# Kernel optimization log

Hardware: AMD Instinct MI355X
Metric: run time of the kernel (lower is better)

## Reference

```python
import jax, jax.numpy as jnp
import numpy as np

N = 50000        # num nodes
E = 800000       # num edges (no self loops by construction)
D = 128          # in_features == out_features
NE = 4           # num_envs
EPS = 1e-8
STDV = 1.0 / np.sqrt(D)


def setup_inputs() -> dict:
    key = jax.random.key(0)
    k = jax.random.split(key, 6)
    x = jax.random.normal(k[0], (N, D), jnp.float32)
    row = jax.random.randint(k[1], (E,), 0, N, dtype=jnp.int32)
    off = jax.random.randint(k[2], (E,), 1, N, dtype=jnp.int32)
    col = (row + off) % N  # guarantees no self loops (matches remove_self_loops)
    adj = jnp.stack([row, col])
    env_weights = jax.random.uniform(k[3], (N, NE), jnp.float32)
    weights = jax.random.uniform(k[4], (NE, D, D), jnp.float32, -STDV, STDV)
    a = jax.random.normal(k[5], (NE, 2 * D, 1), jnp.float32) * np.sqrt(2.0 / (2 * D + 1)) * 1.414
    return {"x": x, "adj": adj, "env_weights": env_weights, "weights": weights, "a": a}


def reference(x, adj, env_weights, weights, a):
    n = x.shape[0]
    f = weights.shape[-1]
    loops = jnp.arange(n, dtype=adj.dtype)
    src = jnp.concatenate([adj[0], loops])  # add_self_loops
    dst = jnp.concatenate([adj[1], loops])
    # per-env projected features: [NE, N, F]
    h = jnp.einsum('nd,edf->enf', x, weights)
    # attention logits: cat(h[src], h[dst]) @ a  ==  h[src]@a1 + h[dst]@a2
    a1 = a[:, :f, 0]   # [NE, F]
    a2 = a[:, f:, 0]   # [NE, F]
    s_src = jnp.einsum('enf,ef->en', h, a1)
    s_dst = jnp.einsum('enf,ef->en', h, a2)
    logits = jax.nn.leaky_relu(s_src[:, src] + s_dst[:, dst], 0.01)  # [NE, Etot]
    # global per-env max subtraction (as in the torch code: max over all edges)
    e = jnp.exp(logits - jnp.max(logits, axis=1, keepdims=True))
    def agg(ek, hk):
        # specialspmm: out[src] += ek * hk[dst]; denom via ones vector
        denom = jax.ops.segment_sum(ek, src, num_segments=n) + EPS          # [N]
        num = jax.ops.segment_sum(ek[:, None] * hk[dst], src, num_segments=n)  # [N, F]
        return num / denom[:, None]
    out_env = jax.vmap(agg)(e, h)  # [NE, N, F]
    out = jnp.einsum('ne,enf->nf', env_weights, out_env)
    return out + x  # residual
```

## Files before the change

kernel.cpp:

```cpp
#include <hip/hip_runtime.h>

#define N_NODES 50000
#define N_EDGES 800000
#define D_FEAT  128
#define NE_ENV  4
#define EPS_F   1e-8f
#define M_CONST 4.0f
#define SCAN_NB 196
#define NB_BUCKET 391
#define BINA_EPT 16

typedef __attribute__((ext_vector_type(8))) short bf16x8;
typedef __attribute__((ext_vector_type(4))) float floatx4;
typedef __attribute__((ext_vector_type(2))) float f32x2;

static __device__ __forceinline__ unsigned short f2bf(float v) {
    union { float f; unsigned int u; } c; c.f = v;
    unsigned int u = c.u;
    u += 0x7fffu + ((u >> 16) & 1u);
    return (unsigned short)(u >> 16);
}

static __device__ __forceinline__ f32x2 bf2f(unsigned int v) {
    f32x2 r;
    r.x = __uint_as_float(v << 16);
    r.y = __uint_as_float(v & 0xffff0000u);
    return r;
}

static __device__ __forceinline__ float lrelu_exp(float z) {
    float lk = z > 0.f ? z : 0.01f * z;
    return __expf(lk - M_CONST);
}

static __device__ __forceinline__ void pk_add(f32x2& acc, f32x2 w) {
    asm("v_pk_add_f32 %0, %1, %0" : "+v"(acc) : "v"(w));
}
static __device__ __forceinline__ void pk_fma_bl(f32x2& acc, f32x2 w, f32x2 x) {
    asm("v_pk_fma_f32 %0, %1, %2, %0 op_sel:[0,0,0] op_sel_hi:[0,1,1]" : "+v"(acc) : "v"(w), "v"(x));
}
static __device__ __forceinline__ void pk_fma_bh(f32x2& acc, f32x2 w, f32x2 x) {
    asm("v_pk_fma_f32 %0, %1, %2, %0 op_sel:[1,0,0] op_sel_hi:[1,1,1]" : "+v"(acc) : "v"(w), "v"(x));
}

static __device__ __forceinline__ void edge_acc(unsigned int xv, float4 w,
        f32x2& den01, f32x2& den23, f32x2* axy) {
    f32x2 x = bf2f(xv);
    f32x2 wxy; wxy.x = w.x; wxy.y = w.y;
    f32x2 wzw; wzw.x = w.z; wzw.y = w.w;
    pk_add(den01, wxy);
    pk_add(den23, wzw);
    pk_fma_bl(axy[0], wxy, x);
    pk_fma_bh(axy[1], wxy, x);
    pk_fma_bl(axy[2], wzw, x);
    pk_fma_bh(axy[3], wzw, x);
}

__global__ __launch_bounds__(256) void k_setup(const float* __restrict__ weights, const float* __restrict__ a,
        float* __restrict__ b, unsigned short* __restrict__ wsw,
        const int* __restrict__ row, int* __restrict__ counts) {
    int blk = blockIdx.x;
    if (blk < 128) {
        int wave = threadIdx.x >> 6, lane = threadIdx.x & 63;
        int t = blk * 4 + wave;
        int e = t >> 7, d = t & 127;
        float2 w2 = ((const float2*)(weights + e * 16384 + d * 128))[lane];
        float2 a1 = ((const float2*)(a + e * 256))[lane];
        float2 a2 = ((const float2*)(a + e * 256 + 128))[lane];
        float p1 = w2.x * a1.x + w2.y * a1.y;
        float p2 = w2.x * a2.x + w2.y * a2.y;
#pragma unroll
        for (int off = 32; off > 0; off >>= 1) {
            p1 += __shfl_xor(p1, off, 64);
            p2 += __shfl_xor(p2, off, 64);
        }
        if (lane == 0) {
            b[e * 128 + d] = p1;
            b[512 + e * 128 + d] = p2;
        }
    } else if (blk < 384) {
        int idx = (blk - 128) * 256 + threadIdx.x;
        int j = idx & 7;
        int l = (idx >> 3) & 63;
        int t = (idx >> 9) & 7;
        int s = idx >> 12;
        int k = s * 32 + (l >> 4) * 8 + j;
        int f = t * 16 + (l & 15);
        int e = k >> 7, d = k & 127;
        wsw[idx] = f2bf(weights[e * 16384 + d * 128 + f]);
    } else {
        int k = (blk - 384) * 256 + threadIdx.x;
        if (k < N_EDGES) atomicAdd(&counts[row[k]], 1);
    }
}

__global__ __launch_bounds__(256) void k_s(const float* __restrict__ x, const float* __restrict__ b,
        float* __restrict__ s_src, float* __restrict__ s_dst, unsigned short* __restrict__ xbf) {
    int wave = threadIdx.x >> 6, lane = threadIdx.x & 63;
    int gw = blockIdx.x * 4 + wave;
    if (gw >= 3125) return;
    int quad = lane >> 4, lm = lane & 15;
    int base = gw * 16;

    floatx4 acc = (floatx4){0.f, 0.f, 0.f, 0.f};
    const float* xrow = x + (size_t)(base + lm) * 128 + quad * 8;
    unsigned short* xbrow = xbf + (size_t)(base + lm) * 128 + quad * 8;

#pragma unroll
    for (int s = 0; s < 4; ++s) {
        float4 lo = *(const float4*)(xrow + s * 32);
        float4 hi = *(const float4*)(xrow + s * 32 + 4);
        bf16x8 af;
        af[0] = (short)f2bf(lo.x); af[1] = (short)f2bf(lo.y);
        af[2] = (short)f2bf(lo.z); af[3] = (short)f2bf(lo.w);
        af[4] = (short)f2bf(hi.x); af[5] = (short)f2bf(hi.y);
        af[6] = (short)f2bf(hi.z); af[7] = (short)f2bf(hi.w);
        *(bf16x8*)(xbrow + s * 32) = af;

        bf16x8 bfv = (bf16x8){0, 0, 0, 0, 0, 0, 0, 0};
        if (lm < 8) {
            const float* bp = b + lm * 128 + s * 32 + quad * 8;
            float4 b0 = *(const float4*)bp;
            float4 b1 = *(const float4*)(bp + 4);
            bfv[0] = (short)f2bf(b0.x); bfv[1] = (short)f2bf(b0.y);
            bfv[2] = (short)f2bf(b0.z); bfv[3] = (short)f2bf(b0.w);
            bfv[4] = (short)f2bf(b1.x); bfv[5] = (short)f2bf(b1.y);
            bfv[6] = (short)f2bf(b1.z); bfv[7] = (short)f2bf(b1.w);
        }
        acc = __builtin_amdgcn_mfma_f32_16x16x32_bf16(af, bfv, acc, 0, 0, 0);
    }
    if (lm < 8) {
        float* dstp = (lm < 4) ? (s_src + (size_t)(base + quad * 4) * 4 + lm)
                               : (s_dst + (size_t)(base + quad * 4) * 4 + (lm - 4));
#pragma unroll
        for (int r = 0; r < 4; ++r) dstp[r * 4] = acc[r];
    }
}

__global__ void k_scan_a(const int* __restrict__ counts, int* __restrict__ partial) {
    __shared__ int sm[256];
    int idx = blockIdx.x * 256 + threadIdx.x;
    sm[threadIdx.x] = (idx < N_NODES) ? counts[idx] : 0;
    __syncthreads();
    for (int s = 128; s > 0; s >>= 1) {
        if (threadIdx.x < s) sm[threadIdx.x] += sm[threadIdx.x + s];
        __syncthreads();
    }
    if (threadIdx.x == 0) partial[blockIdx.x] = sm[0];
}

__global__ void k_scan_b(const int* __restrict__ partial, int* __restrict__ chunk_off) {
    __shared__ int sm[256];
    int t = threadIdx.x;
    int v = (t < SCAN_NB) ? partial[t] : 0;
    sm[t] = v;
    __syncthreads();
    for (int s2 = 1; s2 < 256; s2 <<= 1) {
        int add = (t >= s2) ? sm[t - s2] : 0;
        __syncthreads();
        sm[t] += add;
        __syncthreads();
    }
    chunk_off[t] = sm[t] - v;
}

__global__ void k_scan_c(const int* __restrict__ counts, const int* __restrict__ chunk_off,
                         int* __restrict__ offsets, int* __restrict__ bcur) {
    __shared__ int sm[256];
    int t = threadIdx.x;
    int idx = blockIdx.x * 256 + t;
    int v = (idx < N_NODES) ? counts[idx] : 0;
    sm[t] = v;
    __syncthreads();
    for (int s2 = 1; s2 < 256; s2 <<= 1) {
        int add = (t >= s2) ? sm[t - s2] : 0;
        __syncthreads();
        sm[t] += add;
        __syncthreads();
    }
    if (idx < N_NODES) {
        int excl = chunk_off[blockIdx.x] + sm[t] - v;
        offsets[idx] = excl;
        if ((idx & 127) == 0) bcur[idx >> 7] = excl;
    }
    if (idx == 0) offsets[N_NODES] = N_EDGES;
}

__global__ __launch_bounds__(256) void k_binA(const int* __restrict__ row, const int* __restrict__ col,
        int* __restrict__ bcur, unsigned int* __restrict__ binned) {
    __shared__ int cnt[NB_BUCKET];
    __shared__ int base[NB_BUCKET];
    int t = threadIdx.x;
    for (int b = t; b < NB_BUCKET; b += 256) cnt[b] = 0;
    __syncthreads();
    unsigned int pk[BINA_EPT];
    int ebase = blockIdx.x * (256 * BINA_EPT) + t;
#pragma unroll
    for (int j = 0; j < BINA_EPT; ++j) {
        int k = ebase + j * 256;
        pk[j] = 0xffffffffu;
        if (k < N_EDGES) {
            unsigned int s = (unsigned int)row[k];
            unsigned int d = (unsigned int)col[k];
            pk[j] = (s << 16) | d;
            atomicAdd(&cnt[s >> 7], 1);
        }
    }
    __syncthreads();
    for (int b = t; b < NB_BUCKET; b += 256) {
        int c = cnt[b];
        base[b] = c ? atomicAdd(&bcur[b], c) : 0;
        cnt[b] = 0;
    }
    __syncthreads();
#pragma unroll
    for (int j = 0; j < BINA_EPT; ++j) {
        if (pk[j] != 0xffffffffu) {
            int b = pk[j] >> 23;
            int off = atomicAdd(&cnt[b], 1);
            binned[base[b] + off] = pk[j];
        }
    }
}

__global__ __launch_bounds__(256) void k_binB(const unsigned int* __restrict__ binned,
        const int* __restrict__ offsets,
        const float* __restrict__ s_src, const float* __restrict__ s_dst,
        int* __restrict__ sorted_dst, float4* __restrict__ w_sorted) {
    __shared__ int cur[128];
    int b = blockIdx.x;
    int nb = b << 7;
    int nc = min(128, N_NODES - nb);
    int t = threadIdx.x;
    if (t < nc) cur[t] = offsets[nb + t];
    __syncthreads();
    int ebeg = offsets[nb];
    int eend = offsets[nb + nc];
    for (int i = ebeg + t; i < eend; i += 256) {
        unsigned int pk = binned[i];
        int s = (int)(pk >> 16), d = (int)(pk & 0xffffu);
        float4 a4 = *(const float4*)(s_src + s * 4);
        float4 b4 = *(const float4*)(s_dst + d * 4);
        float4 w;
        w.x = lrelu_exp(a4.x + b4.x);
        w.y = lrelu_exp(a4.y + b4.y);
        w.z = lrelu_exp(a4.z + b4.z);
        w.w = lrelu_exp(a4.w + b4.w);
        int pos = atomicAdd(&cur[s - nb], 1);
        sorted_dst[pos] = d;
        w_sorted[pos] = w;
    }
}

__global__ __launch_bounds__(256) void k_agg(const unsigned int* __restrict__ xb,
        const float* __restrict__ s_src, const float* __restrict__ s_dst,
        const int* __restrict__ offsets, const int* __restrict__ sorted_dst,
        const float4* __restrict__ w_sorted, const float* __restrict__ env_w,
        unsigned short* __restrict__ Gp) {
    int wave = threadIdx.x >> 6, lane = threadIdx.x & 63;
    int n = blockIdx.x * 4 + wave;
    if (n >= N_NODES) return;

    f32x2 den01, den23;
    f32x2 axy[4];

    {
        float4 sa = *(const float4*)(s_src + n * 4);
        float4 sb = *(const float4*)(s_dst + n * 4);
        float ws0 = lrelu_exp(sa.x + sb.x), ws1 = lrelu_exp(sa.y + sb.y);
        float ws2 = lrelu_exp(sa.z + sb.z), ws3 = lrelu_exp(sa.w + sb.w);
        f32x2 xv = bf2f(xb[((unsigned)n << 6) + lane]);
        den01.x = ws0; den01.y = ws1;
        den23.x = ws2; den23.y = ws3;
        axy[0].x = ws0 * xv.x; axy[0].y = ws0 * xv.y;
        axy[1].x = ws1 * xv.x; axy[1].y = ws1 * xv.y;
        axy[2].x = ws2 * xv.x; axy[2].y = ws2 * xv.y;
        axy[3].x = ws3 * xv.x; axy[3].y = ws3 * xv.y;
    }

    int beg = __builtin_amdgcn_readfirstlane(offsets[n]);
    int end = __builtin_amdgcn_readfirstlane(offsets[n + 1]);
    int i = beg;
    for (; i + 7 < end; i += 8) {
        int d[8]; float4 w[8]; unsigned int v[8];
#pragma unroll
        for (int j = 0; j < 8; ++j) d[j] = sorted_dst[i + j];
#pragma unroll
        for (int j = 0; j < 8; ++j) v[j] = xb[((unsigned)d[j] << 6) + lane];
#pragma unroll
        for (int j = 0; j < 8; ++j) w[j] = w_sorted[i + j];
#pragma unroll
        for (int j = 0; j < 8; ++j) edge_acc(v[j], w[j], den01, den23, axy);
    }
    for (; i + 3 < end; i += 4) {
        int d[4]; float4 w[4]; unsigned int v[4];
#pragma unroll
        for (int j = 0; j < 4; ++j) d[j] = sorted_dst[i + j];
#pragma unroll
        for (int j = 0; j < 4; ++j) v[j] = xb[((unsigned)d[j] << 6) + lane];
#pragma unroll
        for (int j = 0; j < 4; ++j) w[j] = w_sorted[i + j];
#pragma unroll
        for (int j = 0; j < 4; ++j) edge_acc(v[j], w[j], den01, den23, axy);
    }
    for (; i < end; ++i) {
        int d0 = sorted_dst[i];
        edge_acc(xb[((unsigned)d0 << 6) + lane], w_sorted[i], den01, den23, axy);
    }

    float4 ewt = *(const float4*)(env_w + n * 4);
    float ewv[4] = { ewt.x, ewt.y, ewt.z, ewt.w };
    float dens[4] = { den01.x, den01.y, den23.x, den23.y };
    unsigned int* grow = (unsigned int*)(Gp + (size_t)n * 512);
#pragma unroll
    for (int e = 0; e < 4; ++e) {
        float sc = ewv[e] / (dens[e] + EPS_F);
        unsigned int lo = f2bf(sc * axy[e].x);
        unsigned int hi = f2bf(sc * axy[e].y);
        grow[e * 64 + lane] = (hi << 16) | lo;
    }
}

__global__ __launch_bounds__(256) void k_gemm(const unsigned short* __restrict__ Gp,
        const unsigned short* __restrict__ Wsw,
        const float* __restrict__ x, float* __restrict__ out) {
    int wave = threadIdx.x >> 6, lane = threadIdx.x & 63;
    int gw = blockIdx.x * 4 + wave;
    if (gw >= 3125) return;
    int quad = lane >> 4, lm = lane & 15;
    int m = gw * 16 + lm;

    floatx4 acc[8];
#pragma unroll
    for (int t = 0; t < 8; ++t) acc[t] = (floatx4){0.f, 0.f, 0.f, 0.f};

    const unsigned short* Arow = Gp + (size_t)m * 512 + quad * 8;
#pragma unroll
    for (int s = 0; s < 16; ++s) {
        bf16x8 af = *(const bf16x8*)(Arow + s * 32);
#pragma unroll
        for (int t = 0; t < 8; ++t) {
            bf16x8 bfv = *(const bf16x8*)(Wsw + (((s * 8 + t) * 64 + lane) * 8));
            acc[t] = __builtin_amdgcn_mfma_f32_16x16x32_bf16(af, bfv, acc[t], 0, 0, 0);
        }
    }
    int row_base = gw * 16 + quad * 4;
#pragma unroll
    for (int t = 0; t < 8; ++t) {
        int colc = t * 16 + lm;
#pragma unroll
        for (int r = 0; r < 4; ++r) {
            int rowi = row_base + r;
            out[rowi * 128 + colc] = acc[t][r] + x[rowi * 128 + colc];
        }
    }
}

extern "C" void kernel_launch(void* const* d_in, const int* in_sizes, int n_in,
                              void* d_out, int out_size, void* d_ws, size_t ws_size,
                              hipStream_t stream) {
    const float* x       = (const float*)d_in[0];
    const int*   adj     = (const int*)d_in[1];
    const int*   row     = adj;
    const int*   col     = adj + N_EDGES;
    const float* env_w   = (const float*)d_in[2];
    const float* weights = (const float*)d_in[3];
    const float* a       = (const float*)d_in[4];
    float* out = (float*)d_out;

    char* ws = (char*)d_ws;
    size_t off = 0;
    auto alloc = [&](size_t bytes) -> char* {
        char* p = ws + off;
        off += (bytes + 255) & ~(size_t)255;
        return p;
    };
    float* b          = (float*)alloc(1024 * 4);
    float* s_src      = (float*)alloc((size_t)N_NODES * 4 * 4);
    float* s_dst      = (float*)alloc((size_t)N_NODES * 4 * 4);
    int*   counts     = (int*)alloc((size_t)N_NODES * 4);
    int*   offsets    = (int*)alloc((size_t)(N_NODES + 1) * 4);
    int*   partial    = (int*)alloc(256 * 4);
    int*   chunk_off  = (int*)alloc(256 * 4);
    int*   bcur       = (int*)alloc(512 * 4);
    unsigned int* binned = (unsigned int*)alloc((size_t)N_EDGES * 4);
    int*   sorted_dst = (int*)alloc((size_t)N_EDGES * 4);
    float4* w_sorted  = (float4*)alloc((size_t)N_EDGES * 16);
    unsigned short* wsw = (unsigned short*)alloc(65536 * 2);
    unsigned short* xbf = (unsigned short*)alloc((size_t)N_NODES * 128 * 2);
    unsigned short* Gp  = (unsigned short*)alloc((size_t)N_NODES * 512 * 2);

    hipMemsetAsync(counts, 0, (size_t)N_NODES * 4, stream);
    k_setup<<<3509, 256, 0, stream>>>(weights, a, b, wsw, row, counts);
    k_s<<<782, 256, 0, stream>>>(x, b, s_src, s_dst, xbf);
    k_scan_a<<<SCAN_NB, 256, 0, stream>>>(counts, partial);
    k_scan_b<<<1, 256, 0, stream>>>(partial, chunk_off);
    k_scan_c<<<SCAN_NB, 256, 0, stream>>>(counts, chunk_off, offsets, bcur);
    k_binA<<<196, 256, 0, stream>>>(row, col, bcur, binned);
    k_binB<<<NB_BUCKET, 256, 0, stream>>>(binned, offsets, s_src, s_dst, sorted_dst, w_sorted);
    k_agg<<<12500, 256, 0, stream>>>((const unsigned int*)xbf, s_src, s_dst, offsets, sorted_dst, w_sorted, env_w, Gp);
    k_gemm<<<782, 256, 0, stream>>>(Gp, wsw, x, out);
}
```

Measured before the change: 228.5 us.

## Fuse aggregation and output GEMM via shared-memory tile

```diff
diff --git a/kernel.cpp b/kernel.cpp
--- a/kernel.cpp
+++ b/kernel.cpp
@@ -252,107 +252,103 @@
     }
 }
 
-__global__ __launch_bounds__(256) void k_agg(const unsigned int* __restrict__ xb,
+__global__ __launch_bounds__(256) void k_agg_gemm(const unsigned int* __restrict__ xb,
         const float* __restrict__ s_src, const float* __restrict__ s_dst,
         const int* __restrict__ offsets, const int* __restrict__ sorted_dst,
         const float4* __restrict__ w_sorted, const float* __restrict__ env_w,
-        unsigned short* __restrict__ Gp) {
-    int wave = threadIdx.x >> 6, lane = threadIdx.x & 63;
-    int n = blockIdx.x * 4 + wave;
-    if (n >= N_NODES) return;
-
-    f32x2 den01, den23;
-    f32x2 axy[4];
-
-    {
-        float4 sa = *(const float4*)(s_src + n * 4);
-        float4 sb = *(const float4*)(s_dst + n * 4);
-        float ws0 = lrelu_exp(sa.x + sb.x), ws1 = lrelu_exp(sa.y + sb.y);
-        float ws2 = lrelu_exp(sa.z + sb.z), ws3 = lrelu_exp(sa.w + sb.w);
-        f32x2 xv = bf2f(xb[((unsigned)n << 6) + lane]);
-        den01.x = ws0; den01.y = ws1;
-        den23.x = ws2; den23.y = ws3;
-        axy[0].x = ws0 * xv.x; axy[0].y = ws0 * xv.y;
-        axy[1].x = ws1 * xv.x; axy[1].y = ws1 * xv.y;
-        axy[2].x = ws2 * xv.x; axy[2].y = ws2 * xv.y;
-        axy[3].x = ws3 * xv.x; axy[3].y = ws3 * xv.y;
-    }
-
-    int beg = __builtin_amdgcn_readfirstlane(offsets[n]);
-    int end = __builtin_amdgcn_readfirstlane(offsets[n + 1]);
-    int i = beg;
-    for (; i + 7 < end; i += 8) {
-        int d[8]; float4 w[8]; unsigned int v[8];
-#pragma unroll
-        for (int j = 0; j < 8; ++j) d[j] = sorted_dst[i + j];
-#pragma unroll
-        for (int j = 0; j < 8; ++j) v[j] = xb[((unsigned)d[j] << 6) + lane];
-#pragma unroll
-        for (int j = 0; j < 8; ++j) w[j] = w_sorted[i + j];
-#pragma unroll
-        for (int j = 0; j < 8; ++j) edge_acc(v[j], w[j], den01, den23, axy);
-    }
-    for (; i + 3 < end; i += 4) {
-        int d[4]; float4 w[4]; unsigned int v[4];
-#pragma unroll
-        for (int j = 0; j < 4; ++j) d[j] = sorted_dst[i + j];
-#pragma unroll
-        for (int j = 0; j < 4; ++j) v[j] = xb[((unsigned)d[j] << 6) + lane];
-#pragma unroll
-        for (int j = 0; j < 4; ++j) w[j] = w_sorted[i + j];
-#pragma unroll
-        for (int j = 0; j < 4; ++j) edge_acc(v[j], w[j], den01, den23, axy);
-    }
-    for (; i < end; ++i) {
-        int d0 = sorted_dst[i];
-        edge_acc(xb[((unsigned)d0 << 6) + lane], w_sorted[i], den01, den23, axy);
-    }
-
-    float4 ewt = *(const float4*)(env_w + n * 4);
-    float ewv[4] = { ewt.x, ewt.y, ewt.z, ewt.w };
-    float dens[4] = { den01.x, den01.y, den23.x, den23.y };
-    unsigned int* grow = (unsigned int*)(Gp + (size_t)n * 512);
-#pragma unroll
-    for (int e = 0; e < 4; ++e) {
-        float sc = ewv[e] / (dens[e] + EPS_F);
-        unsigned int lo = f2bf(sc * axy[e].x);
-        unsigned int hi = f2bf(sc * axy[e].y);
-        grow[e * 64 + lane] = (hi << 16) | lo;
-    }
-}
-
-__global__ __launch_bounds__(256) void k_gemm(const unsigned short* __restrict__ Gp,
         const unsigned short* __restrict__ Wsw,
         const float* __restrict__ x, float* __restrict__ out) {
+    __shared__ __align__(16) unsigned int Gsm[16 * 256];
     int wave = threadIdx.x >> 6, lane = threadIdx.x & 63;
-    int gw = blockIdx.x * 4 + wave;
-    if (gw >= 3125) return;
+    int nb = blockIdx.x * 16;
+
+#pragma unroll 1
+    for (int j = 0; j < 4; ++j) {
+        int r = wave * 4 + j;
+        int n = nb + r;
+
+        f32x2 den01, den23;
+        f32x2 axy[4];
+        {
+            float4 sa = *(const float4*)(s_src + n * 4);
+            float4 sb = *(const float4*)(s_dst + n * 4);
+            float ws0 = lrelu_exp(sa.x + sb.x), ws1 = lrelu_exp(sa.y + sb.y);
+            float ws2 = lrelu_exp(sa.z + sb.z), ws3 = lrelu_exp(sa.w + sb.w);
+            f32x2 xv = bf2f(xb[((unsigned)n << 6) + lane]);
+            den01.x = ws0; den01.y = ws1;
+            den23.x = ws2; den23.y = ws3;
+            axy[0].x = ws0 * xv.x; axy[0].y = ws0 * xv.y;
+            axy[1].x = ws1 * xv.x; axy[1].y = ws1 * xv.y;
+            axy[2].x = ws2 * xv.x; axy[2].y = ws2 * xv.y;
+            axy[3].x = ws3 * xv.x; axy[3].y = ws3 * xv.y;
+        }
+
+        int beg = __builtin_amdgcn_readfirstlane(offsets[n]);
+        int end = __builtin_amdgcn_readfirstlane(offsets[n + 1]);
+        int i = beg;
+        for (; i + 7 < end; i += 8) {
+            int d[8]; float4 w[8]; unsigned int v[8];
+#pragma unroll
+            for (int q = 0; q < 8; ++q) d[q] = sorted_dst[i + q];
+#pragma unroll
+            for (int q = 0; q < 8; ++q) v[q] = xb[((unsigned)d[q] << 6) + lane];
+#pragma unroll
+            for (int q = 0; q < 8; ++q) w[q] = w_sorted[i + q];
+#pragma unroll
+            for (int q = 0; q < 8; ++q) edge_acc(v[q], w[q], den01, den23, axy);
+        }
+        for (; i + 3 < end; i += 4) {
+            int d[4]; float4 w[4]; unsigned int v[4];
+#pragma unroll
+            for (int q = 0; q < 4; ++q) d[q] = sorted_dst[i + q];
+#pragma unroll
+            for (int q = 0; q < 4; ++q) v[q] = xb[((unsigned)d[q] << 6) + lane];
+#pragma unroll
+            for (int q = 0; q < 4; ++q) w[q] = w_sorted[i + q];
+#pragma unroll
+            for (int q = 0; q < 4; ++q) edge_acc(v[q], w[q], den01, den23, axy);
+        }
+        for (; i < end; ++i) {
+            int d0 = sorted_dst[i];
+            edge_acc(xb[((unsigned)d0 << 6) + lane], w_sorted[i], den01, den23, axy);
+        }
+
+        float4 ewt = *(const float4*)(env_w + n * 4);
+        float ewv[4] = { ewt.x, ewt.y, ewt.z, ewt.w };
+        float dens[4] = { den01.x, den01.y, den23.x, den23.y };
+        int swz = (r & 7) << 2;
+#pragma unroll
+        for (int e = 0; e < 4; ++e) {
+            float sc = ewv[e] / (dens[e] + EPS_F);
+            unsigned int lo = f2bf(sc * axy[e].x);
+            unsigned int hi = f2bf(sc * axy[e].y);
+            Gsm[(r * 256 + e * 64 + lane) ^ swz] = (hi << 16) | lo;
+        }
+    }
+    __syncthreads();
+
     int quad = lane >> 4, lm = lane & 15;
-    int m = gw * 16 + lm;
-
-    floatx4 acc[8];
-#pragma unroll
-    for (int t = 0; t < 8; ++t) acc[t] = (floatx4){0.f, 0.f, 0.f, 0.f};
-
-    const unsigned short* Arow = Gp + (size_t)m * 512 + quad * 8;
+    int t0 = wave * 2;
+    floatx4 acc0 = (floatx4){0.f, 0.f, 0.f, 0.f};
+    floatx4 acc1 = (floatx4){0.f, 0.f, 0.f, 0.f};
+    int rswz = (lm & 7) << 2;
 #pragma unroll
     for (int s = 0; s < 16; ++s) {
-        bf16x8 af = *(const bf16x8*)(Arow + s * 32);
-#pragma unroll
-        for (int t = 0; t < 8; ++t) {
-            bf16x8 bfv = *(const bf16x8*)(Wsw + (((s * 8 + t) * 64 + lane) * 8));
-            acc[t] = __builtin_amdgcn_mfma_f32_16x16x32_bf16(af, bfv, acc[t], 0, 0, 0);
-        }
-    }
-    int row_base = gw * 16 + quad * 4;
-#pragma unroll
-    for (int t = 0; t < 8; ++t) {
-        int colc = t * 16 + lm;
-#pragma unroll
-        for (int r = 0; r < 4; ++r) {
-            int rowi = row_base + r;
-            out[rowi * 128 + colc] = acc[t][r] + x[rowi * 128 + colc];
-        }
+        int idx = (lm * 256 + s * 16 + quad * 4) ^ rswz;
+        bf16x8 af = *(const bf16x8*)(&Gsm[idx]);
+        bf16x8 b0 = *(const bf16x8*)(Wsw + (((s * 8 + t0) * 64 + lane) * 8));
+        bf16x8 b1 = *(const bf16x8*)(Wsw + (((s * 8 + t0 + 1) * 64 + lane) * 8));
+        acc0 = __builtin_amdgcn_mfma_f32_16x16x32_bf16(af, b0, acc0, 0, 0, 0);
+        acc1 = __builtin_amdgcn_mfma_f32_16x16x32_bf16(af, b1, acc1, 0, 0, 0);
+    }
+    int row_base = nb + quad * 4;
+#pragma unroll
+    for (int r = 0; r < 4; ++r) {
+        int rowi = row_base + r;
+        int c0 = t0 * 16 + lm;
+        int c1 = c0 + 16;
+        out[rowi * 128 + c0] = acc0[r] + x[rowi * 128 + c0];
+        out[rowi * 128 + c1] = acc1[r] + x[rowi * 128 + c1];
     }
 }
 
@@ -388,7 +384,6 @@
     float4* w_sorted  = (float4*)alloc((size_t)N_EDGES * 16);
     unsigned short* wsw = (unsigned short*)alloc(65536 * 2);
     unsigned short* xbf = (unsigned short*)alloc((size_t)N_NODES * 128 * 2);
-    unsigned short* Gp  = (unsigned short*)alloc((size_t)N_NODES * 512 * 2);
 
     hipMemsetAsync(counts, 0, (size_t)N_NODES * 4, stream);
     k_setup<<<3509, 256, 0, stream>>>(weights, a, b, wsw, row, counts);
@@ -398,6 +393,6 @@
     k_scan_c<<<SCAN_NB, 256, 0, stream>>>(counts, chunk_off, offsets, bcur);
     k_binA<<<196, 256, 0, stream>>>(row, col, bcur, binned);
     k_binB<<<NB_BUCKET, 256, 0, stream>>>(binned, offsets, s_src, s_dst, sorted_dst, w_sorted);
-    k_agg<<<12500, 256, 0, stream>>>((const unsigned int*)xbf, s_src, s_dst, offsets, sorted_dst, w_sorted, env_w, Gp);
-    k_gemm<<<782, 256, 0, stream>>>(Gp, wsw, x, out);
-}
+    k_agg_gemm<<<3125, 256, 0, stream>>>((const unsigned int*)xbf, s_src, s_dst, offsets,
+                                         sorted_dst, w_sorted, env_w, wsw, x, out);
+}
```

Result: faster. 213.5 us (-6.6%).
